# Performance work log

Measured on AMD Instinct MI355X. Metric: run time of the kernel, lower is better.

The kernel has to match this reference:

```python
import jax, jax.numpy as jnp
import numpy as np

NUM_HEADS = 32
NUM_KV_HEADS = 8
HEAD_DIM = 128
WINDOW = 256
NUM_META = 128
ROPE_BASE = 10000.0


def _rope_cos_sin(seq_len, dim, dtype):
    inv_freq = 1.0 / (ROPE_BASE ** (jnp.arange(0, dim, 2, dtype=jnp.float32) / dim))
    pos = jnp.arange(seq_len, dtype=jnp.float32)
    freqs = pos[:, None] * inv_freq[None, :]          # [S, dim/2]
    emb = jnp.concatenate([freqs, freqs], axis=-1)     # [S, dim]
    return emb.astype(dtype) * 0 + jnp.cos(emb).astype(dtype), jnp.sin(emb).astype(dtype)


def _rotate_half(x):
    x1, x2 = jnp.split(x, 2, axis=-1)
    return jnp.concatenate([-x2, x1], axis=-1)


def setup_inputs() -> dict:
    key = jax.random.key(0)
    k1, k2, k3 = jax.random.split(key, 3)
    B, S = 1, 2176
    return {
        "query_states": jax.random.normal(k1, (B, S, NUM_HEADS * HEAD_DIM), dtype=jnp.float32),
        "key_states": jax.random.normal(k2, (B, S, NUM_KV_HEADS * HEAD_DIM), dtype=jnp.float32),
        "value_states": jax.random.normal(k3, (B, S, NUM_KV_HEADS * HEAD_DIM), dtype=jnp.float32),
    }


def reference(query_states, key_states, value_states):
    B, S, _ = query_states.shape
    n_rep = NUM_HEADS // NUM_KV_HEADS

    q = query_states.reshape(B, S, NUM_HEADS, HEAD_DIM).transpose(0, 2, 1, 3)      # [B,H,S,D]
    k = key_states.reshape(B, S, NUM_KV_HEADS, HEAD_DIM).transpose(0, 2, 1, 3)     # [B,Hk,S,D]
    v = value_states.reshape(B, S, NUM_KV_HEADS, HEAD_DIM).transpose(0, 2, 1, 3)

    # GQA expansion: repeat_interleave along head dim
    k = jnp.repeat(k, n_rep, axis=1)   # [B,H,S,D]
    v = jnp.repeat(v, n_rep, axis=1)

    # inline RoPE on q and (expanded) k
    cos, sin = _rope_cos_sin(S, HEAD_DIM, q.dtype)     # [S,D]
    cos = cos[None, None]
    sin = sin[None, None]
    q = q * cos + _rotate_half(q) * sin
    k = k * cos + _rotate_half(k) * sin

    scale = 1.0 / jnp.sqrt(jnp.asarray(HEAD_DIM, q.dtype))
    scores = jnp.einsum("bhqd,bhkd->bhqk", q, k) * scale

    # mask: causal AND (sliding window OR kv is a prefix meta token)
    q_idx = jnp.arange(S)[:, None]
    kv_idx = jnp.arange(S)[None, :]
    causal = q_idx >= kv_idx
    sliding = (q_idx - kv_idx) <= WINDOW
    prefix = kv_idx < NUM_META
    mask = causal & (sliding | prefix)                 # [S,S]

    scores = jnp.where(mask[None, None], scores, jnp.asarray(-jnp.inf, scores.dtype))
    probs = jax.nn.softmax(scores, axis=-1)
    out = jnp.einsum("bhqk,bhkd->bhqd", probs, v)      # [B,H,S,D]
    return out.transpose(0, 2, 1, 3).reshape(B, S, NUM_HEADS * HEAD_DIM)
```

## Files before the change

### kernel.cpp

```cpp
#include <hip/hip_runtime.h>

#define HQ 32
#define HKV 8
#define DH 128
#define WIN 256
#define META 128
#define QSCALE 0.1275174324f
#define NFREQ 0.20762050594046f

typedef __attribute__((ext_vector_type(8))) __bf16 bf16x8;
typedef __attribute__((ext_vector_type(4))) float f32x4;
typedef unsigned short u16;
typedef unsigned int u32;

__device__ __forceinline__ u16 f2bf(float f) {
  u32 u = __float_as_uint(f);
  u += 0x7FFFu + ((u >> 16) & 1u);
  return (u16)(u >> 16);
}
__device__ __forceinline__ u32 packbf(float a, float b) {
  u32 ua = __float_as_uint(a); ua += 0x7FFFu + ((ua >> 16) & 1u);
  u32 ub = __float_as_uint(b); ub += 0x7FFFu + ((ub >> 16) & 1u);
  return (ua >> 16) | (ub & 0xFFFF0000u);
}

__global__ __launch_bounds__(256)
void prep_kv(const float* __restrict__ Kg, const float* __restrict__ Vg,
             u16* __restrict__ Kr, u16* __restrict__ Vt, float2* __restrict__ Tab,
             int S) {
  __shared__ float T[32][132];
  const int hk = blockIdx.x;
  const int s0 = blockIdx.y * 32;
  const int tid = threadIdx.x;
  {
    const int r = tid >> 3, c0 = (tid & 7) * 8;
    const int s = s0 + r;
    const float pos = (float)s;
    const float* src = Kg + ((size_t)s * HKV + hk) * DH;
    u16* dst = Kr + ((size_t)hk * S + s) * DH;
    float x[8], y[8];
    #pragma unroll
    for (int j = 0; j < 8; j += 4) {
      *(float4*)&x[j] = *(const float4*)(src + c0 + j);
      *(float4*)&y[j] = *(const float4*)(src + c0 + 64 + j);
    }
    u16 lo[8], hb[8];
    #pragma unroll
    for (int j = 0; j < 8; ++j) {
      float iv = __builtin_amdgcn_exp2f(-NFREQ * (float)(c0 + j));
      float sv, cv; __sincosf(pos * iv, &sv, &cv);
      if (hk == 0) Tab[(size_t)s * 64 + c0 + j] = make_float2(cv, sv);
      lo[j] = f2bf(x[j] * cv - y[j] * sv);
      hb[j] = f2bf(y[j] * cv + x[j] * sv);
    }
    *(int4*)(dst + c0)      = *(int4*)&lo[0];
    *(int4*)(dst + c0 + 64) = *(int4*)&hb[0];
  }
  {
    const int r = tid >> 3, c = (tid & 7) * 16;
    const float* src = Vg + ((size_t)(s0 + r) * HKV + hk) * DH + c;
    #pragma unroll
    for (int j = 0; j < 16; j += 4) *(float4*)&T[r][c + j] = *(const float4*)(src + j);
  }
  __syncthreads();
  {
    const int d = tid >> 1, hf = (tid & 1) * 16;
    u16 buf[16];
    #pragma unroll
    for (int i = 0; i < 16; ++i) buf[i] = f2bf(T[hf + i][d]);
    u16* dst = Vt + ((size_t)hk * DH + d) * S + s0 + hf;
    *(int4*)(dst)     = *(int4*)&buf[0];
    *(int4*)(dst + 8) = *(int4*)&buf[8];
  }
}

#define LOAD_KV(kv0_) do {                                                 \
    const int4* ks_ = (const int4*)(Kb + (size_t)((kv0_) + kr) * DH + kc); \
    fk0 = ks_[0]; fk1 = ks_[1];                                            \
    const int4* vs_ = (const int4*)(Vb + (kv0_));                          \
    fv0 = vs_[0]; fv1 = vs_[1];                                            \
  } while (0)

#define STORE_KV() do {                                                    \
    *(int4*)&Ks[kr][kc]     = fk0; *(int4*)&Ks[kr][kc + 8] = fk1;          \
    *(int4*)&Vs[vd][vc]     = fv0; *(int4*)&Vs[vd][vc + 8] = fv1;          \
  } while (0)

__global__ __launch_bounds__(512, 4)
void attn_main(const float* __restrict__ Qg, const u16* __restrict__ Kr,
               const u16* __restrict__ Vt, const float2* __restrict__ Tab,
               float* __restrict__ Og, int S) {
  const int h = blockIdx.x;
  const int nqb = gridDim.y;
  const int q0 = (nqb - 1 - (int)blockIdx.y) * 128;
  const int hk = h >> 2;
  const int tid = threadIdx.x;
  const int lane = tid & 63;
  const int wave = tid >> 6;
  const int qid  = lane & 15;
  const int quad = lane >> 4;
  const int k8   = quad * 8;

  __shared__ __align__(16) char smem[54272];
  u16 (*Qs)[136] = (u16(*)[136])smem;
  u16 (*Ks)[136] = (u16(*)[136])smem;
  u16 (*Vs)[72]  = (u16(*)[72])(smem + 17408);
  u16 (*Ps)[72]  = (u16(*)[72])(smem + 35840);

  const u16* Kb = Kr + (size_t)hk * S * DH;
  const int kr = tid >> 3, kc = (tid & 7) * 16;
  const int vd = tid >> 2, vc = (tid & 3) * 16;
  const u16* Vb = Vt + ((size_t)hk * DH + vd) * S + vc;

  int4 fk0, fk1, fv0, fv1;
  LOAD_KV(0);

  {
    const int r = tid >> 2, c0 = (tid & 3) * 16;
    const int s = q0 + r;
    const float* qrow = Qg + ((size_t)s * HQ + h) * DH;
    const float2* tb = Tab + (size_t)s * 64 + c0;
    float x[16], y[16];
    float2 t[16];
    #pragma unroll
    for (int j = 0; j < 16; j += 4) {
      *(float4*)&x[j] = *(const float4*)(qrow + c0 + j);
      *(float4*)&y[j] = *(const float4*)(qrow + c0 + 64 + j);
    }
    #pragma unroll
    for (int j = 0; j < 16; j += 2) *(float4*)&t[j] = *(const float4*)(tb + j);
    u16 lo[16], hb[16];
    #pragma unroll
    for (int j = 0; j < 16; ++j) {
      lo[j] = f2bf((x[j] * t[j].x - y[j] * t[j].y) * QSCALE);
      hb[j] = f2bf((y[j] * t[j].x + x[j] * t[j].y) * QSCALE);
    }
    *(int4*)(&Qs[r][c0])      = *(int4*)&lo[0];
    *(int4*)(&Qs[r][c0 + 8])  = *(int4*)&lo[8];
    *(int4*)(&Qs[r][c0 + 64]) = *(int4*)&hb[0];
    *(int4*)(&Qs[r][c0 + 72]) = *(int4*)&hb[8];
  }
  __syncthreads();
  const int qw0 = q0 + wave * 16;
  const int q   = qw0 + qid;
  bf16x8 qa[4];
  {
    const u16* qb = &Qs[wave * 16 + qid][k8];
    #pragma unroll
    for (int c = 0; c < 4; ++c) qa[c] = *(const bf16x8*)(qb + 32 * c);
  }
  __syncthreads();
  STORE_KV();
  __syncthreads();

  int wstart = q0 - WIN; if (wstart < META) wstart = META;
  int nwin = (q0 + 128 - wstart) >> 6; if (nwin < 0) nwin = 0;
  const int ntiles = 2 + nwin;

  f32x4 acc[8];
  #pragma unroll
  for (int D = 0; D < 8; ++D)
    #pragma unroll
    for (int r = 0; r < 4; ++r) acc[D][r] = 0.f;
  float m_i = -1e30f, l_i = 0.f;

  for (int t = 0; t < ntiles; ++t) {
    const int kv0 = (t < 2) ? t * 64 : wstart + (t - 2) * 64;
    const bool haveNext = (t + 1 < ntiles);
    if (haveNext) {
      const int kvn = (t + 1 < 2) ? (t + 1) * 64 : wstart + (t - 1) * 64;
      LOAD_KV(kvn);
    }

    const bool active = (kv0 <= qw0 + 15) &&
                        ((kv0 < META) || (qw0 - kv0 - 63 <= WIN));
    if (active) {
      f32x4 sv[4];
      #pragma unroll
      for (int T = 0; T < 4; ++T)
        #pragma unroll
        for (int r = 0; r < 4; ++r) sv[T][r] = 0.f;
      #pragma unroll
      for (int T = 0; T < 4; ++T) {
        const u16* ka = &Ks[16 * T + qid][k8];
        #pragma unroll
        for (int c = 0; c < 4; ++c)
          sv[T] = __builtin_amdgcn_mfma_f32_16x16x32_bf16(
                    *(const bf16x8*)(ka + 32 * c), qa[c], sv[T], 0, 0, 0);
      }

      const bool fullv = (kv0 + 63 <= qw0) &&
                         ((kv0 + 63 < META) || (qw0 + 15 - kv0 <= WIN));
      if (!fullv) {
        #pragma unroll
        for (int T = 0; T < 4; ++T) {
          #pragma unroll
          for (int r = 0; r < 4; ++r) {
            const int kv = kv0 + 16 * T + 4 * quad + r;
            if (!((kv <= q) && (((q - kv) <= WIN) || (kv < META)))) sv[T][r] = -1e30f;
          }
        }
      }

      float mx = -1e30f;
      #pragma unroll
      for (int T = 0; T < 4; ++T)
        #pragma unroll
        for (int r = 0; r < 4; ++r) mx = fmaxf(mx, sv[T][r]);
      mx = fmaxf(mx, __shfl_xor(mx, 16));
      mx = fmaxf(mx, __shfl_xor(mx, 32));
      const float mnew = fmaxf(m_i, mx);
      const float al = __builtin_amdgcn_exp2f(m_i - mnew);
      m_i = mnew;
      float ps = 0.f;
      #pragma unroll
      for (int T = 0; T < 4; ++T)
        #pragma unroll
        for (int r = 0; r < 4; ++r) {
          sv[T][r] = __builtin_amdgcn_exp2f(sv[T][r] - mnew);
          ps += sv[T][r];
        }
      l_i = l_i * al + ps;
      #pragma unroll
      for (int D = 0; D < 8; ++D)
        #pragma unroll
        for (int r = 0; r < 4; ++r) acc[D][r] *= al;

      {
        int2* pw = (int2*)&Ps[wave * 16 + qid][0];
        #pragma unroll
        for (int T = 0; T < 4; ++T) {
          int2 pr;
          pr.x = (int)packbf(sv[T][0], sv[T][1]);
          pr.y = (int)packbf(sv[T][2], sv[T][3]);
          pw[4 * T + quad] = pr;
        }
      }
      const u16* pb = &Ps[wave * 16 + qid][k8];
      const bf16x8 p0 = *(const bf16x8*)(pb);
      const bf16x8 p1 = *(const bf16x8*)(pb + 32);

      #pragma unroll
      for (int D = 0; D < 8; ++D) {
        const u16* va = &Vs[16 * D + qid][k8];
        acc[D] = __builtin_amdgcn_mfma_f32_16x16x32_bf16(*(const bf16x8*)(va),      p0, acc[D], 0, 0, 0);
        acc[D] = __builtin_amdgcn_mfma_f32_16x16x32_bf16(*(const bf16x8*)(va + 32), p1, acc[D], 0, 0, 0);
      }
    }

    if (haveNext) {
      __syncthreads();
      STORE_KV();
      __syncthreads();
    }
  }

  l_i += __shfl_xor(l_i, 16);
  l_i += __shfl_xor(l_i, 32);
  const float inv = 1.0f / l_i;
  float* ob = Og + ((size_t)q * HQ + h) * DH;
  #pragma unroll
  for (int D = 0; D < 8; ++D) {
    float4 o = { acc[D][0] * inv, acc[D][1] * inv, acc[D][2] * inv, acc[D][3] * inv };
    *(float4*)(ob + 16 * D + 4 * quad) = o;
  }
}

extern "C" void kernel_launch(void* const* d_in, const int* in_sizes, int n_in,
                              void* d_out, int out_size, void* d_ws, size_t ws_size,
                              hipStream_t stream) {
  const float* Qg = (const float*)d_in[0];
  const float* Kg = (const float*)d_in[1];
  const float* Vg = (const float*)d_in[2];
  float* Og = (float*)d_out;
  const int S = in_sizes[0] / (HQ * DH);

  u16* Kr = (u16*)d_ws;
  u16* Vt = (u16*)((char*)d_ws + (size_t)HKV * S * DH * 2);
  float2* Tab = (float2*)((char*)d_ws + (size_t)HKV * S * DH * 4);

  prep_kv<<<dim3(HKV, S / 32), dim3(256), 0, stream>>>(Kg, Vg, Kr, Vt, Tab, S);
  attn_main<<<dim3(HQ, S / 128), dim3(512), 0, stream>>>(Qg, Kr, Vt, Tab, Og, S);
}
```

Measured before the change: 137.4 us.

## Halve attention query tile, read K from global directly, use hardware sincos

The attention kernel now processes 64 query rows per block with 256 threads instead of 128 rows with 512, doubling the grid for more parallelism. K tiles are no longer staged in shared memory; each wave loads K fragments straight from global (relying on cache), so LDS holds only Q, the V tile and P, which shrinks shared memory. RoPE in the prep kernel uses the hardware sin/cos instructions on a fract-reduced angle. Risks: more redundant window-tile loads per query row, uncached-global latency on the QK MFMAs, and slightly lower precision for the angle reduction.

```diff
diff --git a/kernel.cpp b/kernel.cpp
--- a/kernel.cpp
+++ b/kernel.cpp
@@ -7,6 +7,7 @@
 #define META 128
 #define QSCALE 0.1275174324f
 #define NFREQ 0.20762050594046f
+#define INV2PI 0.15915494309189535f
 
 typedef __attribute__((ext_vector_type(8))) __bf16 bf16x8;
 typedef __attribute__((ext_vector_type(4))) float f32x4;
@@ -22,6 +23,12 @@
   u32 ua = __float_as_uint(a); ua += 0x7FFFu + ((ua >> 16) & 1u);
   u32 ub = __float_as_uint(b); ub += 0x7FFFu + ((ub >> 16) & 1u);
   return (ua >> 16) | (ub & 0xFFFF0000u);
+}
+
+__device__ __forceinline__ void hw_sincos(float pos, float iv_rev, float* s, float* c) {
+  float a = __builtin_amdgcn_fractf(pos * iv_rev);
+  *s = __builtin_amdgcn_sinf(a);
+  *c = __builtin_amdgcn_cosf(a);
 }
 
 __global__ __launch_bounds__(256)
@@ -47,8 +54,8 @@
     u16 lo[8], hb[8];
     #pragma unroll
     for (int j = 0; j < 8; ++j) {
-      float iv = __builtin_amdgcn_exp2f(-NFREQ * (float)(c0 + j));
-      float sv, cv; __sincosf(pos * iv, &sv, &cv);
+      float iv = __builtin_amdgcn_exp2f(-NFREQ * (float)(c0 + j)) * INV2PI;
+      float sv, cv; hw_sincos(pos, iv, &sv, &cv);
       if (hk == 0) Tab[(size_t)s * 64 + c0 + j] = make_float2(cv, sv);
       lo[j] = f2bf(x[j] * cv - y[j] * sv);
       hb[j] = f2bf(y[j] * cv + x[j] * sv);
@@ -74,25 +81,23 @@
   }
 }
 
-#define LOAD_KV(kv0_) do {                                                 \
-    const int4* ks_ = (const int4*)(Kb + (size_t)((kv0_) + kr) * DH + kc); \
-    fk0 = ks_[0]; fk1 = ks_[1];                                            \
+#define LOAD_V(kv0_) do {                                                  \
     const int4* vs_ = (const int4*)(Vb + (kv0_));                          \
-    fv0 = vs_[0]; fv1 = vs_[1];                                            \
+    fv0 = vs_[0]; fv1 = vs_[1]; fv2 = vs_[2]; fv3 = vs_[3];                \
   } while (0)
 
-#define STORE_KV() do {                                                    \
-    *(int4*)&Ks[kr][kc]     = fk0; *(int4*)&Ks[kr][kc + 8] = fk1;          \
-    *(int4*)&Vs[vd][vc]     = fv0; *(int4*)&Vs[vd][vc + 8] = fv1;          \
+#define STORE_V() do {                                                     \
+    int4* vd_ = (int4*)&Vs[tid >> 1][(tid & 1) * 32];                      \
+    vd_[0] = fv0; vd_[1] = fv1; vd_[2] = fv2; vd_[3] = fv3;                \
   } while (0)
 
-__global__ __launch_bounds__(512, 4)
+__global__ __launch_bounds__(256, 4)
 void attn_main(const float* __restrict__ Qg, const u16* __restrict__ Kr,
                const u16* __restrict__ Vt, const float2* __restrict__ Tab,
                float* __restrict__ Og, int S) {
   const int h = blockIdx.x;
   const int nqb = gridDim.y;
-  const int q0 = (nqb - 1 - (int)blockIdx.y) * 128;
+  const int q0 = (nqb - 1 - (int)blockIdx.y) * 64;
   const int hk = h >> 2;
   const int tid = threadIdx.x;
   const int lane = tid & 63;
@@ -101,19 +106,16 @@
   const int quad = lane >> 4;
   const int k8   = quad * 8;
 
-  __shared__ __align__(16) char smem[54272];
+  __shared__ __align__(16) char smem[27648];
   u16 (*Qs)[136] = (u16(*)[136])smem;
-  u16 (*Ks)[136] = (u16(*)[136])smem;
-  u16 (*Vs)[72]  = (u16(*)[72])(smem + 17408);
-  u16 (*Ps)[72]  = (u16(*)[72])(smem + 35840);
-
-  const u16* Kb = Kr + (size_t)hk * S * DH;
-  const int kr = tid >> 3, kc = (tid & 7) * 16;
-  const int vd = tid >> 2, vc = (tid & 3) * 16;
-  const u16* Vb = Vt + ((size_t)hk * DH + vd) * S + vc;
-
-  int4 fk0, fk1, fv0, fv1;
-  LOAD_KV(0);
+  u16 (*Vs)[72]  = (u16(*)[72])smem;
+  u16 (*Ps)[72]  = (u16(*)[72])(smem + 18432);
+
+  const u16* Kq = Kr + (size_t)hk * S * DH + (size_t)qid * DH + k8;
+  const u16* Vb = Vt + ((size_t)hk * DH + (tid >> 1)) * S + (tid & 1) * 32;
+
+  int4 fv0, fv1, fv2, fv3;
+  LOAD_V(0);
 
   {
     const int r = tid >> 2, c0 = (tid & 3) * 16;
@@ -150,11 +152,11 @@
     for (int c = 0; c < 4; ++c) qa[c] = *(const bf16x8*)(qb + 32 * c);
   }
   __syncthreads();
-  STORE_KV();
+  STORE_V();
   __syncthreads();
 
   int wstart = q0 - WIN; if (wstart < META) wstart = META;
-  int nwin = (q0 + 128 - wstart) >> 6; if (nwin < 0) nwin = 0;
+  int nwin = (q0 + 64 - wstart) >> 6; if (nwin < 0) nwin = 0;
   const int ntiles = 2 + nwin;
 
   f32x4 acc[8];
@@ -169,12 +171,13 @@
     const bool haveNext = (t + 1 < ntiles);
     if (haveNext) {
       const int kvn = (t + 1 < 2) ? (t + 1) * 64 : wstart + (t - 1) * 64;
-      LOAD_KV(kvn);
+      LOAD_V(kvn);
     }
 
     const bool active = (kv0 <= qw0 + 15) &&
                         ((kv0 < META) || (qw0 - kv0 - 63 <= WIN));
     if (active) {
+      const u16* kt = Kq + (size_t)kv0 * DH;
       f32x4 sv[4];
       #pragma unroll
       for (int T = 0; T < 4; ++T)
@@ -182,11 +185,15 @@
         for (int r = 0; r < 4; ++r) sv[T][r] = 0.f;
       #pragma unroll
       for (int T = 0; T < 4; ++T) {
-        const u16* ka = &Ks[16 * T + qid][k8];
-        #pragma unroll
-        for (int c = 0; c < 4; ++c)
-          sv[T] = __builtin_amdgcn_mfma_f32_16x16x32_bf16(
-                    *(const bf16x8*)(ka + 32 * c), qa[c], sv[T], 0, 0, 0);
+        const u16* kp = kt + (size_t)T * 16 * DH;
+        int4 kA = *(const int4*)(kp);
+        int4 kB = *(const int4*)(kp + 32);
+        int4 kC = *(const int4*)(kp + 64);
+        int4 kD = *(const int4*)(kp + 96);
+        sv[T] = __builtin_amdgcn_mfma_f32_16x16x32_bf16(*(const bf16x8*)&kA, qa[0], sv[T], 0, 0, 0);
+        sv[T] = __builtin_amdgcn_mfma_f32_16x16x32_bf16(*(const bf16x8*)&kB, qa[1], sv[T], 0, 0, 0);
+        sv[T] = __builtin_amdgcn_mfma_f32_16x16x32_bf16(*(const bf16x8*)&kC, qa[2], sv[T], 0, 0, 0);
+        sv[T] = __builtin_amdgcn_mfma_f32_16x16x32_bf16(*(const bf16x8*)&kD, qa[3], sv[T], 0, 0, 0);
       }
 
       const bool fullv = (kv0 + 63 <= qw0) &&
@@ -250,7 +257,7 @@
 
     if (haveNext) {
       __syncthreads();
-      STORE_KV();
+      STORE_V();
       __syncthreads();
     }
   }
@@ -280,5 +287,5 @@
   float2* Tab = (float2*)((char*)d_ws + (size_t)HKV * S * DH * 4);
 
   prep_kv<<<dim3(HKV, S / 32), dim3(256), 0, stream>>>(Kg, Vg, Kr, Vt, Tab, S);
-  attn_main<<<dim3(HQ, S / 128), dim3(512), 0, stream>>>(Qg, Kr, Vt, Tab, Og, S);
-}
+  attn_main<<<dim3(HQ, S / 64), dim3(256), 0, stream>>>(Qg, Kr, Vt, Tab, Og, S);
+}
```

New measurement: 170.1 us. 1.24x slower.

## Halve attention query tile, add lazy softmax rescale and hardware sincos

Applied to the files above, without the earlier changes.

The attention kernel now processes 64 query rows per block with 256 threads instead of 128 rows with 512, so the grid has twice as many smaller blocks. K/V staging loads are widened to 64 bytes per thread to cover the tile with fewer threads. Online softmax skips rescaling the accumulators unless the running max grows by more than 8 in the log2 domain. RoPE sin/cos now use hardware fract/sin/cos. The changes aim to cut masked-out work and rescale multiplies and to improve occupancy and load balance, at the cost of more K/V reloads per query and slightly lower trig precision.

```diff
diff --git a/kernel.cpp b/kernel.cpp
--- a/kernel.cpp
+++ b/kernel.cpp
@@ -7,6 +7,7 @@
 #define META 128
 #define QSCALE 0.1275174324f
 #define NFREQ 0.20762050594046f
+#define INV2PI 0.15915494309189535f
 
 typedef __attribute__((ext_vector_type(8))) __bf16 bf16x8;
 typedef __attribute__((ext_vector_type(4))) float f32x4;
@@ -22,6 +23,11 @@
   u32 ua = __float_as_uint(a); ua += 0x7FFFu + ((ua >> 16) & 1u);
   u32 ub = __float_as_uint(b); ub += 0x7FFFu + ((ub >> 16) & 1u);
   return (ua >> 16) | (ub & 0xFFFF0000u);
+}
+__device__ __forceinline__ void hw_sincos(float pos, float iv_rev, float* s, float* c) {
+  float a = __builtin_amdgcn_fractf(pos * iv_rev);
+  *s = __builtin_amdgcn_sinf(a);
+  *c = __builtin_amdgcn_cosf(a);
 }
 
 __global__ __launch_bounds__(256)
@@ -47,8 +53,8 @@
     u16 lo[8], hb[8];
     #pragma unroll
     for (int j = 0; j < 8; ++j) {
-      float iv = __builtin_amdgcn_exp2f(-NFREQ * (float)(c0 + j));
-      float sv, cv; __sincosf(pos * iv, &sv, &cv);
+      float iv = __builtin_amdgcn_exp2f(-NFREQ * (float)(c0 + j)) * INV2PI;
+      float sv, cv; hw_sincos(pos, iv, &sv, &cv);
       if (hk == 0) Tab[(size_t)s * 64 + c0 + j] = make_float2(cv, sv);
       lo[j] = f2bf(x[j] * cv - y[j] * sv);
       hb[j] = f2bf(y[j] * cv + x[j] * sv);
@@ -76,23 +82,25 @@
 
 #define LOAD_KV(kv0_) do {                                                 \
     const int4* ks_ = (const int4*)(Kb + (size_t)((kv0_) + kr) * DH + kc); \
-    fk0 = ks_[0]; fk1 = ks_[1];                                            \
+    fk0 = ks_[0]; fk1 = ks_[1]; fk2 = ks_[2]; fk3 = ks_[3];                \
     const int4* vs_ = (const int4*)(Vb + (kv0_));                          \
-    fv0 = vs_[0]; fv1 = vs_[1];                                            \
+    fv0 = vs_[0]; fv1 = vs_[1]; fv2 = vs_[2]; fv3 = vs_[3];                \
   } while (0)
 
 #define STORE_KV() do {                                                    \
-    *(int4*)&Ks[kr][kc]     = fk0; *(int4*)&Ks[kr][kc + 8] = fk1;          \
-    *(int4*)&Vs[vd][vc]     = fv0; *(int4*)&Vs[vd][vc + 8] = fv1;          \
+    int4* kd_ = (int4*)&Ks[kr][kc];                                        \
+    kd_[0] = fk0; kd_[1] = fk1; kd_[2] = fk2; kd_[3] = fk3;                \
+    int4* vd_ = (int4*)&Vs[tid >> 1][(tid & 1) * 32];                      \
+    vd_[0] = fv0; vd_[1] = fv1; vd_[2] = fv2; vd_[3] = fv3;                \
   } while (0)
 
-__global__ __launch_bounds__(512, 4)
+__global__ __launch_bounds__(256, 3)
 void attn_main(const float* __restrict__ Qg, const u16* __restrict__ Kr,
                const u16* __restrict__ Vt, const float2* __restrict__ Tab,
                float* __restrict__ Og, int S) {
   const int h = blockIdx.x;
   const int nqb = gridDim.y;
-  const int q0 = (nqb - 1 - (int)blockIdx.y) * 128;
+  const int q0 = (nqb - 1 - (int)blockIdx.y) * 64;
   const int hk = h >> 2;
   const int tid = threadIdx.x;
   const int lane = tid & 63;
@@ -101,18 +109,17 @@
   const int quad = lane >> 4;
   const int k8   = quad * 8;
 
-  __shared__ __align__(16) char smem[54272];
+  __shared__ __align__(16) char smem[45056];
   u16 (*Qs)[136] = (u16(*)[136])smem;
   u16 (*Ks)[136] = (u16(*)[136])smem;
   u16 (*Vs)[72]  = (u16(*)[72])(smem + 17408);
   u16 (*Ps)[72]  = (u16(*)[72])(smem + 35840);
 
   const u16* Kb = Kr + (size_t)hk * S * DH;
-  const int kr = tid >> 3, kc = (tid & 7) * 16;
-  const int vd = tid >> 2, vc = (tid & 3) * 16;
-  const u16* Vb = Vt + ((size_t)hk * DH + vd) * S + vc;
-
-  int4 fk0, fk1, fv0, fv1;
+  const u16* Vb = Vt + ((size_t)hk * DH + (tid >> 1)) * S + (tid & 1) * 32;
+  const int kr = tid >> 2, kc = (tid & 3) * 32;
+
+  int4 fk0, fk1, fk2, fk3, fv0, fv1, fv2, fv3;
   LOAD_KV(0);
 
   {
@@ -154,7 +161,7 @@
   __syncthreads();
 
   int wstart = q0 - WIN; if (wstart < META) wstart = META;
-  int nwin = (q0 + 128 - wstart) >> 6; if (nwin < 0) nwin = 0;
+  int nwin = (q0 + 64 - wstart) >> 6; if (nwin < 0) nwin = 0;
   const int ntiles = 2 + nwin;
 
   f32x4 acc[8];
@@ -209,22 +216,25 @@
         for (int r = 0; r < 4; ++r) mx = fmaxf(mx, sv[T][r]);
       mx = fmaxf(mx, __shfl_xor(mx, 16));
       mx = fmaxf(mx, __shfl_xor(mx, 32));
-      const float mnew = fmaxf(m_i, mx);
-      const float al = __builtin_amdgcn_exp2f(m_i - mnew);
-      m_i = mnew;
+      if (!__all(mx - m_i <= 8.0f)) {
+        const float mnew = fmaxf(m_i, mx);
+        const float al = __builtin_amdgcn_exp2f(m_i - mnew);
+        m_i = mnew;
+        l_i *= al;
+        #pragma unroll
+        for (int D = 0; D < 8; ++D)
+          #pragma unroll
+          for (int r = 0; r < 4; ++r) acc[D][r] *= al;
+      }
       float ps = 0.f;
       #pragma unroll
       for (int T = 0; T < 4; ++T)
         #pragma unroll
         for (int r = 0; r < 4; ++r) {
-          sv[T][r] = __builtin_amdgcn_exp2f(sv[T][r] - mnew);
+          sv[T][r] = __builtin_amdgcn_exp2f(sv[T][r] - m_i);
           ps += sv[T][r];
         }
-      l_i = l_i * al + ps;
-      #pragma unroll
-      for (int D = 0; D < 8; ++D)
-        #pragma unroll
-        for (int r = 0; r < 4; ++r) acc[D][r] *= al;
+      l_i += ps;
 
       {
         int2* pw = (int2*)&Ps[wave * 16 + qid][0];
@@ -280,5 +290,5 @@
   float2* Tab = (float2*)((char*)d_ws + (size_t)HKV * S * DH * 4);
 
   prep_kv<<<dim3(HKV, S / 32), dim3(256), 0, stream>>>(Kg, Vg, Kr, Vt, Tab, S);
-  attn_main<<<dim3(HQ, S / 128), dim3(512), 0, stream>>>(Qg, Kr, Vt, Tab, Og, S);
-}
+  attn_main<<<dim3(HQ, S / 64), dim3(256), 0, stream>>>(Qg, Kr, Vt, Tab, Og, S);
+}
```

Measured after the change: 135.0 us. No clear change (-1.8%).
